# Optimization experiments

Measured on AMD Instinct MI355X. Metric: run time of the kernel, lower is better.

The kernel has to match this reference:

```python
import jax, jax.numpy as jnp
import numpy as np

SEQ_LEN = 8192
VOCAB = 128000
EMB = 10   # embedding_size hard-coded in RNNLM.__init__
HID = 10   # hidden_size hard-coded


def setup_inputs() -> dict:
    key = jax.random.key(0)
    k1, k2, k3, k4, k5, k6 = jax.random.split(key, 6)
    input_batch = jax.random.randint(k1, (SEQ_LEN, 1), 0, VOCAB, dtype=jnp.int32)
    embedding = jax.random.normal(k2, (VOCAB, EMB), dtype=jnp.float32)
    # nn.Linear(input+hidden -> hidden) and nn.Linear(input+hidden -> vocab)
    W_i2h = jax.random.normal(k3, (HID, EMB + HID), dtype=jnp.float32) * 0.1
    b_i2h = jax.random.normal(k4, (HID,), dtype=jnp.float32) * 0.1
    W_i2o = jax.random.normal(k5, (VOCAB, EMB + HID), dtype=jnp.float32) * 0.1
    b_i2o = jax.random.normal(k6, (VOCAB,), dtype=jnp.float32) * 0.1
    return {
        "input_batch": input_batch,
        "embedding": embedding,
        "W_i2h": W_i2h,
        "b_i2h": b_i2h,
        "W_i2o": W_i2o,
        "b_i2o": b_i2o,
    }


def reference(input_batch, embedding, W_i2h, b_i2h, W_i2o, b_i2o):
    # Elman RNN unrolled over time via lax.scan; batch is 1 (required by the
    # original torch.cat of [B,10] embedding with [1,10] hidden state).
    def step(hidden, word_ix):
        w = embedding[word_ix]                              # (1, EMB)
        combined = jnp.concatenate([w, hidden], axis=1)     # (1, EMB+HID)
        new_hidden = combined @ W_i2h.T + b_i2h             # (1, HID)
        logits = combined @ W_i2o.T + b_i2o                 # (1, VOCAB)
        logp = jax.nn.log_softmax(logits, axis=1)
        pred = jnp.argmax(logp, axis=1).astype(jnp.float32)  # topk(1) index
        return new_hidden, pred

    hidden0 = jnp.zeros((1, HID), dtype=jnp.float32)
    _, preds = jax.lax.scan(step, hidden0, input_batch)     # preds: (SEQ_LEN, 1)
    return preds
```

## Files before the change

kernel.cpp:

```cpp
#include <hip/hip_runtime.h>

#define SEQ   8192
#define VOCAB 128000
#define L     64
#define NCH   128

#define OFF_CMB    0
#define OFF_CVEC   163840
#define OFF_AMAX   245760
#define OFF_AMAX1  262144
#define OFF_CNORM  270336
#define OFF_WPART  278528
#define OFF_WMAX   279040
#define OFF_C32    279104
#define OFF_W32    410176

#define TBLK   16
#define VSL2   125
#define VSPAN  1024
#define NIT    32
#define SEEDSL 32
#define CCAP   4096

typedef __attribute__((ext_vector_type(8))) short bf16x8;
typedef __attribute__((ext_vector_type(4))) float f32x4;

static __device__ inline unsigned short f2bf(float x) {
    unsigned u = __float_as_uint(x);
    u += 0x7FFF + ((u >> 16) & 1);
    return (unsigned short)(u >> 16);
}
static __device__ inline unsigned sortable(float x) {
    unsigned u = __float_as_uint(x);
    return (u & 0x80000000u) ? ~u : (u | 0x80000000u);
}
static __device__ inline float unsortable(unsigned k) {
    unsigned u = (k & 0x80000000u) ? (k & 0x7FFFFFFFu) : ~k;
    return __uint_as_float(u);
}

__global__ void k_prep(const int* __restrict__ ix, const float* __restrict__ emb,
                       const float* __restrict__ Wih, const float* __restrict__ bih,
                       const float* __restrict__ Wio, const float* __restrict__ bio,
                       float* __restrict__ ws) {
    int b = blockIdx.x;
    int tid = threadIdx.x;
    if (b < 32) {
        int t = b * 256 + tid;
        ((unsigned long long*)(ws + OFF_AMAX))[t] = 0ULL;
        ((unsigned*)(ws + OFF_AMAX1))[t] = 0u;

        int id = ix[t];
        float w[10];
        const float2* ep = (const float2*)(emb + (long long)id * 10);
#pragma unroll
        for (int j = 0; j < 5; j++) ((float2*)w)[j] = ep[j];
#pragma unroll
        for (int j = 0; j < 10; j++) ws[OFF_CMB + j * SEQ + t] = w[j];

        int m = t >> 6, k = t & 63;
        float* cv = ws + OFF_CVEC + (k * NCH + m) * 10;
#pragma unroll
        for (int i = 0; i < 10; i++) {
            float s = bih[i];
#pragma unroll
            for (int j = 0; j < 10; j++) s += Wih[i * 20 + j] * w[j];
            cv[i] = s;
        }
    } else {
        __shared__ float red[4];
        int bs = b - 32;
        int v = bs * 256 + tid;
        float w[20];
        const float4* r = (const float4*)(Wio + (long long)v * 20);
#pragma unroll
        for (int q = 0; q < 5; q++) ((float4*)w)[q] = r[q];
        float bv = bio[v];
        float n2 = bv * bv;
#pragma unroll
        for (int k = 0; k < 20; k++) n2 += w[k] * w[k];
        float nrm = sqrtf(n2);
        for (int off = 1; off < 64; off <<= 1)
            nrm = fmaxf(nrm, __shfl_xor(nrm, off));
        if ((tid & 63) == 0) red[tid >> 6] = nrm;
        __syncthreads();
        if (tid == 0)
            ws[OFF_WPART + bs] = fmaxf(fmaxf(red[0], red[1]), fmaxf(red[2], red[3]));

        unsigned short h[32];
#pragma unroll
        for (int k = 0; k < 20; k++) h[k] = f2bf(w[k]);
        h[20] = f2bf(bv);
#pragma unroll
        for (int k = 21; k < 32; k++) h[k] = 0;
        uint4* dst = (uint4*)((unsigned short*)(ws + OFF_W32));
#pragma unroll
        for (int i = 0; i < 4; i++) {
            uint4 u;
            u.x = (unsigned)h[8*i+0] | ((unsigned)h[8*i+1] << 16);
            u.y = (unsigned)h[8*i+2] | ((unsigned)h[8*i+3] << 16);
            u.z = (unsigned)h[8*i+4] | ((unsigned)h[8*i+5] << 16);
            u.w = (unsigned)h[8*i+6] | ((unsigned)h[8*i+7] << 16);
            dst[v * 4 + i] = u;
        }
    }
}

__global__ void k_scan(const float* __restrict__ Wih, float* __restrict__ ws) {
    __shared__ float P[100], Q[100];
    __shared__ float Dl[NCH][10];
    __shared__ float Hst[NCH][10];
    __shared__ float Hl[10];
    int tid = threadIdx.x;

    float Ar[10][10];
#pragma unroll
    for (int i = 0; i < 10; i++)
#pragma unroll
        for (int j = 0; j < 10; j++) Ar[i][j] = Wih[i * 20 + 10 + j];

    {
        int m = tid;
        float h[10];
#pragma unroll
        for (int i = 0; i < 10; i++) h[i] = 0.f;
        const float* cvb = ws + OFF_CVEC;
        float2 buf[5];
        {
            const float2* cp = (const float2*)(cvb + m * 10);
#pragma unroll
            for (int j = 0; j < 5; j++) buf[j] = cp[j];
        }
        for (int k = 0; k < L; k++) {
            float cc[10];
#pragma unroll
            for (int j = 0; j < 5; j++) { cc[2*j] = buf[j].x; cc[2*j+1] = buf[j].y; }
            if (k + 1 < L) {
                const float2* cp = (const float2*)(cvb + ((k + 1) * NCH + m) * 10);
#pragma unroll
                for (int j = 0; j < 5; j++) buf[j] = cp[j];
            }
            float nh[10];
#pragma unroll
            for (int i = 0; i < 10; i++) {
                float s = cc[i];
#pragma unroll
                for (int j = 0; j < 10; j++) s += Ar[i][j] * h[j];
                nh[i] = s;
            }
#pragma unroll
            for (int i = 0; i < 10; i++) h[i] = nh[i];
        }
#pragma unroll
        for (int i = 0; i < 10; i++) Dl[m][i] = h[i];
    }

    if (tid < 100) P[tid] = Wih[(tid / 10) * 20 + 10 + (tid % 10)];
    __syncthreads();
    for (int it = 0; it < 6; it++) {
        if (tid < 100) {
            int i = tid / 10, j = tid % 10;
            float s = 0.f;
#pragma unroll
            for (int k = 0; k < 10; k++) s += P[i * 10 + k] * P[k * 10 + j];
            Q[tid] = s;
        }
        __syncthreads();
        if (tid < 100) P[tid] = Q[tid];
        __syncthreads();
    }

    if (tid < 10) Hl[tid] = 0.f;
    __syncthreads();
    if (tid < 10) {
        int i = tid;
        float a64[10];
#pragma unroll
        for (int j = 0; j < 10; j++) a64[j] = P[i * 10 + j];
        float hc = 0.f;
        for (int m = 0; m < NCH; m++) {
            Hst[m][i] = hc;
            float s = Dl[m][i];
#pragma unroll
            for (int j = 0; j < 10; j++) s += a64[j] * Hl[j];
            Hl[i] = s;
            hc = s;
        }
    }
    __syncthreads();

    {
        int m = tid;
        float h[10];
#pragma unroll
        for (int i = 0; i < 10; i++) h[i] = Hst[m][i];
        const float* cvb = ws + OFF_CVEC;
        float2 buf[5];
        {
            const float2* cp = (const float2*)(cvb + m * 10);
#pragma unroll
            for (int j = 0; j < 5; j++) buf[j] = cp[j];
        }
        for (int k = 0; k < L; k++) {
            int tg = m * 64 + k;
            float cc[10];
#pragma unroll
            for (int j = 0; j < 5; j++) { cc[2*j] = buf[j].x; cc[2*j+1] = buf[j].y; }
            if (k + 1 < L) {
                const float2* cp = (const float2*)(cvb + ((k + 1) * NCH + m) * 10);
#pragma unroll
                for (int j = 0; j < 5; j++) buf[j] = cp[j];
            }
#pragma unroll
            for (int i = 0; i < 10; i++) ws[OFF_CMB + (10 + i) * SEQ + tg] = h[i];
            float nh[10];
#pragma unroll
            for (int i = 0; i < 10; i++) {
                float s = cc[i];
#pragma unroll
                for (int j = 0; j < 10; j++) s += Ar[i][j] * h[j];
                nh[i] = s;
            }
#pragma unroll
            for (int i = 0; i < 10; i++) h[i] = nh[i];
        }
    }
}

__global__ void k_pack_c(float* __restrict__ ws) {
    int b = blockIdx.x;
    int tid = threadIdx.x;
    if (b == 32) {
        __shared__ float red[4];
        float m = 0.f;
        for (int i = tid; i < 500; i += 256) m = fmaxf(m, ws[OFF_WPART + i]);
        for (int off = 1; off < 64; off <<= 1)
            m = fmaxf(m, __shfl_xor(m, off));
        if ((tid & 63) == 0) red[tid >> 6] = m;
        __syncthreads();
        if (tid == 0)
            ws[OFF_WMAX] = fmaxf(fmaxf(red[0], red[1]), fmaxf(red[2], red[3]));
        return;
    }
    int t = b * 256 + tid;
    float c[20];
#pragma unroll
    for (int k = 0; k < 20; k++) c[k] = ws[OFF_CMB + k * SEQ + t];
    float n2 = 1.0f;
#pragma unroll
    for (int k = 0; k < 20; k++) n2 += c[k] * c[k];
    ws[OFF_CNORM + t] = sqrtf(n2);

    unsigned short h[32];
#pragma unroll
    for (int k = 0; k < 20; k++) h[k] = f2bf(c[k]);
    h[20] = f2bf(1.0f);
#pragma unroll
    for (int k = 21; k < 32; k++) h[k] = 0;
    uint4* dst = (uint4*)((unsigned short*)(ws + OFF_C32));
#pragma unroll
    for (int i = 0; i < 4; i++) {
        uint4 u;
        u.x = (unsigned)h[8*i+0] | ((unsigned)h[8*i+1] << 16);
        u.y = (unsigned)h[8*i+2] | ((unsigned)h[8*i+3] << 16);
        u.z = (unsigned)h[8*i+4] | ((unsigned)h[8*i+5] << 16);
        u.w = (unsigned)h[8*i+6] | ((unsigned)h[8*i+7] << 16);
        dst[t * 4 + i] = u;
    }
}

__global__ __launch_bounds__(256, 4)
void k_seed(const float* __restrict__ ws, unsigned* __restrict__ amax1) {
    int tid = threadIdx.x;
    int lane = tid & 63, wid = tid >> 6, quad = lane >> 4, col = lane & 15;
    int tb  = blockIdx.x >> 5;
    int sl  = blockIdx.x & 31;
    int t0w = tb * 512 + wid * 128;
    int v0s = sl * VSPAN;

    const unsigned short* c32 = (const unsigned short*)(ws + OFF_C32);
    const unsigned short* Wg  = (const unsigned short*)(ws + OFF_W32);

    bf16x8 a[8];
#pragma unroll
    for (int tt = 0; tt < 8; tt++)
        a[tt] = *(const bf16x8*)(c32 + (t0w + tt * 16 + col) * 32 + quad * 8);

    const f32x4 zero = {0.f, 0.f, 0.f, 0.f};
    float run[8][4];
#pragma unroll
    for (int tt = 0; tt < 8; tt++)
#pragma unroll
        for (int g = 0; g < 4; g++) run[tt][g] = -3.4e38f;

    const unsigned short* Wb = Wg + (unsigned)(v0s + col) * 32 + quad * 8;
    bf16x8 nb0 = *(const bf16x8*)(Wb);
    bf16x8 nb1 = *(const bf16x8*)(Wb + 512);

    for (int p = 0; p < NIT; ++p) {
        bf16x8 b0 = nb0, b1 = nb1;
        if (p + 1 < NIT) {
            const unsigned short* Wn = Wb + (p + 1) * 1024;
            nb0 = *(const bf16x8*)(Wn);
            nb1 = *(const bf16x8*)(Wn + 512);
        }
#pragma unroll
        for (int tt = 0; tt < 8; tt++) {
            f32x4 d0 = __builtin_amdgcn_mfma_f32_16x16x32_bf16(a[tt], b0, zero, 0, 0, 0);
            f32x4 d1 = __builtin_amdgcn_mfma_f32_16x16x32_bf16(a[tt], b1, zero, 0, 0, 0);
#pragma unroll
            for (int g = 0; g < 4; g++)
                run[tt][g] = fmaxf(run[tt][g], fmaxf(d0[g], d1[g]));
        }
    }

#pragma unroll
    for (int tt = 0; tt < 8; tt++)
#pragma unroll
        for (int g = 0; g < 4; g++) {
            float r = run[tt][g];
            for (int off = 1; off < 16; off <<= 1)
                r = fmaxf(r, __shfl_xor(r, off));
            if (col == 0)
                atomicMax(&amax1[t0w + tt * 16 + quad * 4 + g], sortable(r));
        }
}

__global__ __launch_bounds__(256, 4)
void k_cand(const float* __restrict__ ws, const float* __restrict__ Wio,
            const float* __restrict__ bio, const unsigned* __restrict__ amax1,
            unsigned long long* __restrict__ amax) {
    __shared__ unsigned cand[CCAP];
    __shared__ unsigned cnt;

    int tid = threadIdx.x;
    int lane = tid & 63, wid = tid >> 6, quad = lane >> 4, col = lane & 15;
    int tb  = blockIdx.x & 15;
    int sl  = blockIdx.x >> 4;
    int t0w = tb * 512 + wid * 128;
    int v0s = sl * VSPAN;
    if (tid == 0) cnt = 0;
    __syncthreads();

    const unsigned short* c32 = (const unsigned short*)(ws + OFF_C32);
    const unsigned short* Wg  = (const unsigned short*)(ws + OFF_W32);
    float wmax = ws[OFF_WMAX];

    bf16x8 a[8];
    float thr[8][4], thrmin[8];
#pragma unroll
    for (int tt = 0; tt < 8; tt++) {
        a[tt] = *(const bf16x8*)(c32 + (t0w + tt * 16 + col) * 32 + quad * 8);
        float mn = 3.4e38f;
#pragma unroll
        for (int g = 0; g < 4; g++) {
            int t = t0w + tt * 16 + quad * 4 + g;
            float maxap = unsortable(amax1[t]);
            thr[tt][g] = maxap - (0.04f * ws[OFF_CNORM + t] * wmax + 1e-5f);
            mn = fminf(mn, thr[tt][g]);
        }
        thrmin[tt] = mn;
    }

    const f32x4 zero = {0.f, 0.f, 0.f, 0.f};
    const unsigned short* Wb = Wg + (unsigned)(v0s + col) * 32 + quad * 8;
    bf16x8 nb0 = *(const bf16x8*)(Wb);
    bf16x8 nb1 = *(const bf16x8*)(Wb + 512);

    for (int p = 0; p < NIT; ++p) {
        bf16x8 b0 = nb0, b1 = nb1;
        if (p + 1 < NIT) {
            const unsigned short* Wn = Wb + (p + 1) * 1024;
            nb0 = *(const bf16x8*)(Wn);
            nb1 = *(const bf16x8*)(Wn + 512);
        }
        int v0 = v0s + p * 32 + col;
#pragma unroll
        for (int tt = 0; tt < 8; tt++) {
            f32x4 d0 = __builtin_amdgcn_mfma_f32_16x16x32_bf16(a[tt], b0, zero, 0, 0, 0);
            f32x4 d1 = __builtin_amdgcn_mfma_f32_16x16x32_bf16(a[tt], b1, zero, 0, 0, 0);
            float h0 = fmaxf(fmaxf(d0[0], d1[0]), fmaxf(d0[1], d1[1]));
            float h1 = fmaxf(fmaxf(d0[2], d1[2]), fmaxf(d0[3], d1[3]));
            float hm = fmaxf(h0, h1);
            if (hm >= thrmin[tt]) {
#pragma unroll
                for (int g = 0; g < 4; g++) {
                    unsigned t = (unsigned)(t0w + tt * 16 + quad * 4 + g);
                    if (d0[g] >= thr[tt][g]) {
                        unsigned idx = atomicAdd(&cnt, 1u);
                        if (idx < CCAP) cand[idx] = (t << 17) | (unsigned)v0;
                    }
                    if (d1[g] >= thr[tt][g]) {
                        unsigned idx = atomicAdd(&cnt, 1u);
                        if (idx < CCAP) cand[idx] = (t << 17) | (unsigned)(v0 + 16);
                    }
                }
            }
        }
    }

    __syncthreads();
    unsigned n = cnt < CCAP ? cnt : CCAP;
    const float* cmb = ws + OFF_CMB;
    for (unsigned i = tid; i < n; i += 256) {
        unsigned e = cand[i];
        int t = (int)(e >> 17);
        int v = (int)(e & 0x1FFFFu);
        const float* wr = Wio + (long long)v * 20;
        float ex = bio[v];
#pragma unroll
        for (int k = 0; k < 20; k++)
            ex = fmaf(wr[k], cmb[k * SEQ + t], ex);
        unsigned key = sortable(ex);
        unsigned long long packed =
            ((unsigned long long)key << 32) | (unsigned)(VOCAB - v);
        unsigned long long cur = amax[t];
        if (packed > cur)
            atomicMax(&amax[t], packed);
    }
}

__global__ void k_out(const unsigned long long* __restrict__ amax,
                      float* __restrict__ out) {
    int t = blockIdx.x * blockDim.x + threadIdx.x;
    if (t >= SEQ) return;
    unsigned long long p = amax[t];
    int idx = VOCAB - (int)(p & 0xFFFFFFFFu);
    out[t] = (float)idx;
}

extern "C" void kernel_launch(void* const* d_in, const int* in_sizes, int n_in,
                              void* d_out, int out_size, void* d_ws, size_t ws_size,
                              hipStream_t stream) {
    (void)in_sizes; (void)n_in; (void)out_size; (void)ws_size;
    const int*   ix  = (const int*)d_in[0];
    const float* emb = (const float*)d_in[1];
    const float* Wih = (const float*)d_in[2];
    const float* bih = (const float*)d_in[3];
    const float* Wio = (const float*)d_in[4];
    const float* bio = (const float*)d_in[5];
    float* out = (float*)d_out;
    float* ws  = (float*)d_ws;
    unsigned long long* amax = (unsigned long long*)(ws + OFF_AMAX);
    unsigned* amax1 = (unsigned*)(ws + OFF_AMAX1);

    hipLaunchKernelGGL(k_prep,   dim3(532),           dim3(256), 0, stream, ix, emb, Wih, bih, Wio, bio, ws);
    hipLaunchKernelGGL(k_scan,   dim3(1),             dim3(128), 0, stream, Wih, ws);
    hipLaunchKernelGGL(k_pack_c, dim3(33),            dim3(256), 0, stream, ws);
    hipLaunchKernelGGL(k_seed,   dim3(TBLK * SEEDSL), dim3(256), 0, stream, ws, amax1);
    hipLaunchKernelGGL(k_cand,   dim3(TBLK * VSL2),   dim3(256), 0, stream, ws, Wio, bio, amax1, amax);
    hipLaunchKernelGGL(k_out,    dim3(SEQ / 256),     dim3(256), 0, stream, amax, out);
}
```

Measured before the change: 346.9 us.

## Defer candidate extraction to a bitmask pass and widen seed grid

After: 300.6 us. -13.4%, faster.

```diff
diff --git a/kernel.cpp b/kernel.cpp
--- a/kernel.cpp
+++ b/kernel.cpp
@@ -19,6 +19,7 @@
 #define VSL2   125
 #define VSPAN  1024
 #define NIT    32
+#define SEEDTB 32
 #define SEEDSL 32
 #define CCAP   4096
 
@@ -275,21 +276,21 @@
     int lane = tid & 63, wid = tid >> 6, quad = lane >> 4, col = lane & 15;
     int tb  = blockIdx.x >> 5;
     int sl  = blockIdx.x & 31;
-    int t0w = tb * 512 + wid * 128;
+    int t0w = tb * 256 + wid * 64;
     int v0s = sl * VSPAN;
 
     const unsigned short* c32 = (const unsigned short*)(ws + OFF_C32);
     const unsigned short* Wg  = (const unsigned short*)(ws + OFF_W32);
 
-    bf16x8 a[8];
-#pragma unroll
-    for (int tt = 0; tt < 8; tt++)
+    bf16x8 a[4];
+#pragma unroll
+    for (int tt = 0; tt < 4; tt++)
         a[tt] = *(const bf16x8*)(c32 + (t0w + tt * 16 + col) * 32 + quad * 8);
 
     const f32x4 zero = {0.f, 0.f, 0.f, 0.f};
-    float run[8][4];
-#pragma unroll
-    for (int tt = 0; tt < 8; tt++)
+    float run[4][4];
+#pragma unroll
+    for (int tt = 0; tt < 4; tt++)
 #pragma unroll
         for (int g = 0; g < 4; g++) run[tt][g] = -3.4e38f;
 
@@ -299,13 +300,12 @@
 
     for (int p = 0; p < NIT; ++p) {
         bf16x8 b0 = nb0, b1 = nb1;
-        if (p + 1 < NIT) {
-            const unsigned short* Wn = Wb + (p + 1) * 1024;
-            nb0 = *(const bf16x8*)(Wn);
-            nb1 = *(const bf16x8*)(Wn + 512);
-        }
-#pragma unroll
-        for (int tt = 0; tt < 8; tt++) {
+        int pn = (p + 1 < NIT) ? p + 1 : p;
+        const unsigned short* Wn = Wb + pn * 1024;
+        nb0 = *(const bf16x8*)(Wn);
+        nb1 = *(const bf16x8*)(Wn + 512);
+#pragma unroll
+        for (int tt = 0; tt < 4; tt++) {
             f32x4 d0 = __builtin_amdgcn_mfma_f32_16x16x32_bf16(a[tt], b0, zero, 0, 0, 0);
             f32x4 d1 = __builtin_amdgcn_mfma_f32_16x16x32_bf16(a[tt], b1, zero, 0, 0, 0);
 #pragma unroll
@@ -315,7 +315,7 @@
     }
 
 #pragma unroll
-    for (int tt = 0; tt < 8; tt++)
+    for (int tt = 0; tt < 4; tt++)
 #pragma unroll
         for (int g = 0; g < 4; g++) {
             float r = run[tt][g];
@@ -347,19 +347,16 @@
     float wmax = ws[OFF_WMAX];
 
     bf16x8 a[8];
-    float thr[8][4], thrmin[8];
+    float thr[8][4];
 #pragma unroll
     for (int tt = 0; tt < 8; tt++) {
         a[tt] = *(const bf16x8*)(c32 + (t0w + tt * 16 + col) * 32 + quad * 8);
-        float mn = 3.4e38f;
 #pragma unroll
         for (int g = 0; g < 4; g++) {
             int t = t0w + tt * 16 + quad * 4 + g;
             float maxap = unsortable(amax1[t]);
             thr[tt][g] = maxap - (0.04f * ws[OFF_CNORM + t] * wmax + 1e-5f);
-            mn = fminf(mn, thr[tt][g]);
-        }
-        thrmin[tt] = mn;
+        }
     }
 
     const f32x4 zero = {0.f, 0.f, 0.f, 0.f};
@@ -367,33 +364,55 @@
     bf16x8 nb0 = *(const bf16x8*)(Wb);
     bf16x8 nb1 = *(const bf16x8*)(Wb + 512);
 
+    unsigned mask[8];
+#pragma unroll
+    for (int tt = 0; tt < 8; tt++) mask[tt] = 0u;
+
     for (int p = 0; p < NIT; ++p) {
         bf16x8 b0 = nb0, b1 = nb1;
-        if (p + 1 < NIT) {
-            const unsigned short* Wn = Wb + (p + 1) * 1024;
-            nb0 = *(const bf16x8*)(Wn);
-            nb1 = *(const bf16x8*)(Wn + 512);
-        }
-        int v0 = v0s + p * 32 + col;
+        int pn = (p + 1 < NIT) ? p + 1 : p;
+        const unsigned short* Wn = Wb + pn * 1024;
+        nb0 = *(const bf16x8*)(Wn);
+        nb1 = *(const bf16x8*)(Wn + 512);
+        unsigned bit = 1u << p;
 #pragma unroll
         for (int tt = 0; tt < 8; tt++) {
             f32x4 d0 = __builtin_amdgcn_mfma_f32_16x16x32_bf16(a[tt], b0, zero, 0, 0, 0);
             f32x4 d1 = __builtin_amdgcn_mfma_f32_16x16x32_bf16(a[tt], b1, zero, 0, 0, 0);
-            float h0 = fmaxf(fmaxf(d0[0], d1[0]), fmaxf(d0[1], d1[1]));
-            float h1 = fmaxf(fmaxf(d0[2], d1[2]), fmaxf(d0[3], d1[3]));
-            float hm = fmaxf(h0, h1);
-            if (hm >= thrmin[tt]) {
-#pragma unroll
-                for (int g = 0; g < 4; g++) {
-                    unsigned t = (unsigned)(t0w + tt * 16 + quad * 4 + g);
-                    if (d0[g] >= thr[tt][g]) {
-                        unsigned idx = atomicAdd(&cnt, 1u);
-                        if (idx < CCAP) cand[idx] = (t << 17) | (unsigned)v0;
-                    }
-                    if (d1[g] >= thr[tt][g]) {
-                        unsigned idx = atomicAdd(&cnt, 1u);
-                        if (idx < CCAP) cand[idx] = (t << 17) | (unsigned)(v0 + 16);
-                    }
+            unsigned hit = 0u;
+#pragma unroll
+            for (int g = 0; g < 4; g++) {
+                float mg = fmaxf(d0[g], d1[g]);
+                hit |= (mg >= thr[tt][g]) ? bit : 0u;
+            }
+            mask[tt] |= hit;
+        }
+    }
+
+#pragma unroll
+    for (int tt = 0; tt < 8; tt++) {
+        unsigned m = mask[tt];
+        for (int off = 1; off < 64; off <<= 1)
+            m |= __shfl_xor(m, off);
+        while (m) {
+            int p = __ffs(m) - 1;
+            m &= m - 1;
+            const unsigned short* Wp = Wb + p * 1024;
+            bf16x8 b0 = *(const bf16x8*)(Wp);
+            bf16x8 b1 = *(const bf16x8*)(Wp + 512);
+            f32x4 d0 = __builtin_amdgcn_mfma_f32_16x16x32_bf16(a[tt], b0, zero, 0, 0, 0);
+            f32x4 d1 = __builtin_amdgcn_mfma_f32_16x16x32_bf16(a[tt], b1, zero, 0, 0, 0);
+            int v0 = v0s + p * 32 + col;
+#pragma unroll
+            for (int g = 0; g < 4; g++) {
+                unsigned t = (unsigned)(t0w + tt * 16 + quad * 4 + g);
+                if (d0[g] >= thr[tt][g]) {
+                    unsigned idx = atomicAdd(&cnt, 1u);
+                    if (idx < CCAP) cand[idx] = (t << 17) | (unsigned)v0;
+                }
+                if (d1[g] >= thr[tt][g]) {
+                    unsigned idx = atomicAdd(&cnt, 1u);
+                    if (idx < CCAP) cand[idx] = (t << 17) | (unsigned)(v0 + 16);
                 }
             }
         }
@@ -444,10 +463,10 @@
     unsigned long long* amax = (unsigned long long*)(ws + OFF_AMAX);
     unsigned* amax1 = (unsigned*)(ws + OFF_AMAX1);
 
-    hipLaunchKernelGGL(k_prep,   dim3(532),           dim3(256), 0, stream, ix, emb, Wih, bih, Wio, bio, ws);
-    hipLaunchKernelGGL(k_scan,   dim3(1),             dim3(128), 0, stream, Wih, ws);
-    hipLaunchKernelGGL(k_pack_c, dim3(33),            dim3(256), 0, stream, ws);
-    hipLaunchKernelGGL(k_seed,   dim3(TBLK * SEEDSL), dim3(256), 0, stream, ws, amax1);
-    hipLaunchKernelGGL(k_cand,   dim3(TBLK * VSL2),   dim3(256), 0, stream, ws, Wio, bio, amax1, amax);
-    hipLaunchKernelGGL(k_out,    dim3(SEQ / 256),     dim3(256), 0, stream, amax, out);
-}
+    hipLaunchKernelGGL(k_prep,   dim3(532),             dim3(256), 0, stream, ix, emb, Wih, bih, Wio, bio, ws);
+    hipLaunchKernelGGL(k_scan,   dim3(1),               dim3(128), 0, stream, Wih, ws);
+    hipLaunchKernelGGL(k_pack_c, dim3(33),              dim3(256), 0, stream, ws);
+    hipLaunchKernelGGL(k_seed,   dim3(SEEDTB * SEEDSL), dim3(256), 0, stream, ws, amax1);
+    hipLaunchKernelGGL(k_cand,   dim3(TBLK * VSL2),     dim3(256), 0, stream, ws, Wio, bio, amax1, amax);
+    hipLaunchKernelGGL(k_out,    dim3(SEQ / 256),       dim3(256), 0, stream, amax, out);
+}
```
